# Optimization experiments

Measured on AMD Instinct MI355X. Metric: run time of the kernel, lower is better.

The kernel has to match this reference:

```python
import jax, jax.numpy as jnp
import numpy as np

H, KVH, HD = 16, 8, 64
EPS = 1e-6
SCALING = HD ** -0.5


def _rms_norm(x, w):
    # RMSNorm over last dim (head_dim)
    var = jnp.mean(x * x, axis=-1, keepdims=True)
    return x * jax.lax.rsqrt(var + EPS) * w


def _rotate_half(x):
    x1, x2 = jnp.split(x, 2, axis=-1)
    return jnp.concatenate([-x2, x1], axis=-1)


def setup_inputs() -> dict:
    key = jax.random.key(0)
    ks = jax.random.split(key, 12)
    B, Q, CTX, HID = 1, 2048, 2048, 1024
    NB, T = 32, 64  # Q == NB * T
    TOTAL = CTX + Q
    inp = {}
    inp["hidden_states"] = jax.random.normal(ks[0], (B, Q, HID), jnp.float32)
    inp["target_hidden"] = jax.random.normal(ks[1], (B, CTX, HID), jnp.float32)
    pos = jnp.arange(TOTAL, dtype=jnp.float32)[:, None]
    inv = 1.0 / (10000.0 ** (jnp.arange(0, HD, 2, dtype=jnp.float32) / HD))
    ang = pos * inv[None, :]
    emb = jnp.concatenate([ang, ang], axis=-1)
    inp["cos"] = jnp.cos(emb)[None]  # [B, TOTAL, HD]
    inp["sin"] = jnp.sin(emb)[None]
    inp["attention_mask"] = jnp.zeros((B, 1, Q, TOTAL), jnp.float32)
    s = 0.02
    inp["Wq"] = jax.random.normal(ks[2], (HID, H * HD), jnp.float32) * s
    inp["Wk"] = jax.random.normal(ks[3], (HID, KVH * HD), jnp.float32) * s
    inp["Wv"] = jax.random.normal(ks[4], (HID, KVH * HD), jnp.float32) * s
    inp["Wo"] = jax.random.normal(ks[5], (H * HD, HID), jnp.float32) * s
    inp["q_norm_w"] = jnp.ones((HD,), jnp.float32)
    inp["k_norm_w"] = jnp.ones((HD,), jnp.float32)
    inp["tree_bias"] = jax.random.normal(ks[6], (64, H), jnp.float32) * s
    inp["relation_map"] = jax.random.randint(ks[7], (B, NB, T, T), 0, 64, jnp.int32)
    return inp


def reference(hidden_states, target_hidden, cos, sin, attention_mask,
              Wq, Wk, Wv, Wo, q_norm_w, k_norm_w, tree_bias, relation_map):
    B, Q, HID = hidden_states.shape
    CTX = target_hidden.shape[1]
    TOTAL = CTX + Q
    NB, T = relation_map.shape[1], relation_map.shape[2]
    groups = H // KVH

    q = (hidden_states @ Wq).reshape(B, Q, H, HD)
    k_ctx = target_hidden @ Wk
    k_noise = hidden_states @ Wk
    v_ctx = target_hidden @ Wv
    v_noise = hidden_states @ Wv
    k = jnp.concatenate([k_ctx, k_noise], axis=1).reshape(B, TOTAL, KVH, HD)
    v = jnp.concatenate([v_ctx, v_noise], axis=1).reshape(B, TOTAL, KVH, HD)

    q = _rms_norm(q, q_norm_w).transpose(0, 2, 1, 3)  # [B,H,Q,HD]
    k = _rms_norm(k, k_norm_w).transpose(0, 2, 1, 3)  # [B,KVH,TOTAL,HD]
    v = v.transpose(0, 2, 1, 3)

    cos_b = cos[:, None]  # [B,1,TOTAL,HD]
    sin_b = sin[:, None]
    q = q * cos_b[..., -Q:, :] + _rotate_half(q) * sin_b[..., -Q:, :]
    k = k * cos_b + _rotate_half(k) * sin_b

    # GQA: repeat kv heads
    k = jnp.repeat(k, groups, axis=1)  # [B,H,TOTAL,HD]
    v = jnp.repeat(v, groups, axis=1)

    scores = jnp.einsum('bhqd,bhkd->bhqk', q, k) * SCALING  # [B,H,Q,TOTAL]
    scores = scores + attention_mask

    # tree positional bias: block-diagonal (same tree) on the noise-noise block
    bias = tree_bias[relation_map]                 # [B,NB,T,T,H]
    bias = jnp.transpose(bias, (0, 4, 1, 2, 3))    # [B,H,NB,T,T]
    s_noise = scores[..., CTX:].reshape(B, H, NB, T, NB, T)
    idx = jnp.arange(NB)
    s_noise = s_noise.at[:, :, idx, :, idx, :].add(jnp.transpose(bias, (2, 0, 1, 3, 4)))
    scores = jnp.concatenate([scores[..., :CTX], s_noise.reshape(B, H, Q, Q)], axis=-1)

    attn = jax.nn.softmax(scores, axis=-1)
    out = jnp.einsum('bhqk,bhkd->bhqd', attn, v)   # [B,H,Q,HD]
    out = out.transpose(0, 2, 1, 3).reshape(B, Q, H * HD)
    return out @ Wo
```

## Files before the change

kernel.cpp:

```cpp
#include <hip/hip_runtime.h>
#include <hip/hip_bf16.h>

typedef __bf16 bf16x8 __attribute__((ext_vector_type(8)));
typedef float  f32x4  __attribute__((ext_vector_type(4)));

__device__ inline unsigned short f2bf(float f) {
    unsigned int u = __float_as_uint(f);
    u += 0x7fffu + ((u >> 16) & 1u);
    return (unsigned short)(u >> 16);
}
__device__ inline float bf2f(unsigned int s) {
    return __uint_as_float(s << 16);
}
__device__ inline unsigned int pk2bf(float a, float b) {
    __hip_bfloat162 h = __float22bfloat162_rn(make_float2(a, b));
    union { __hip_bfloat162 h; unsigned int u; } cv;
    cv.h = h;
    return cv.u;
}
__device__ inline f32x4 mfma16(bf16x8 a, bf16x8 b, f32x4 c) {
    return __builtin_amdgcn_mfma_f32_16x16x32_bf16(a, b, c, 0, 0, 0);
}
__device__ inline void gload_lds16(const void* g, void* l) {
    __builtin_amdgcn_global_load_lds(
        (const __attribute__((address_space(1))) void*)g,
        (__attribute__((address_space(3))) void*)l, 16, 0, 0);
}

__global__ __launch_bounds__(256) void prep1(const float* __restrict__ th, const float* __restrict__ hs,
                                             const float* __restrict__ Wk, const float* __restrict__ Wv,
                                             const float* __restrict__ Wq, const float* __restrict__ Wo,
                                             unsigned short* __restrict__ X,
                                             unsigned short* __restrict__ Wkvt,
                                             unsigned short* __restrict__ Wqt,
                                             unsigned short* __restrict__ Wot) {
    __shared__ float t[64][65];
    int bx = blockIdx.x, tid = threadIdx.x;
    if (bx < 4096) {
        int i = bx * 256 + tid;
        const int n4 = 2048 * 1024 / 4;
        float4 v = (i < n4) ? ((const float4*)th)[i] : ((const float4*)hs)[i - n4];
        ((uint2*)X)[i] = make_uint2(pk2bf(v.x, v.y), pk2bf(v.z, v.w));
        return;
    }
    int t4 = bx - 4096;
    const float* in; unsigned short* out; int in_rs, xt, yt;
    if (t4 < 256)      { in = Wq; out = Wqt; in_rs = 1024; xt = t4 & 15; yt = t4 >> 4; }
    else if (t4 < 512) { t4 -= 256; in = Wo; out = Wot; in_rs = 1024; xt = t4 & 15; yt = t4 >> 4; }
    else if (t4 < 640) { t4 -= 512; in = Wk; out = Wkvt; in_rs = 512; xt = t4 & 7; yt = t4 >> 3; }
    else               { t4 -= 640; in = Wv; out = Wkvt + (size_t)512 * 1024; in_rs = 512; xt = t4 & 7; yt = t4 >> 3; }
    int r0 = yt * 64, c0b = xt * 64;
    int rr = tid >> 4, c4 = (tid & 15) * 4;
#pragma unroll
    for (int i = 0; i < 4; i++) {
        int r = rr + 16 * i;
        float4 v = *(const float4*)&in[(size_t)(r0 + r) * in_rs + c0b + c4];
        t[c4][r] = v.x; t[c4 + 1][r] = v.y; t[c4 + 2][r] = v.z; t[c4 + 3][r] = v.w;
    }
    __syncthreads();
#pragma unroll
    for (int i = 0; i < 4; i++) {
        int cc = rr + 16 * i;
        *(uint2*)&out[(size_t)(c0b + cc) * 1024 + r0 + c4] =
            make_uint2(pk2bf(t[cc][c4], t[cc][c4 + 1]), pk2bf(t[cc][c4 + 2], t[cc][c4 + 3]));
    }
}

union GemmLds {
    struct { unsigned short A[2][128 * 64]; unsigned short B[2][64 * 64]; } s;
    unsigned short Ost[128 * 72];
};

__device__ __forceinline__ void gemm_bk64(const unsigned short* __restrict__ A,
                                          const unsigned short* __restrict__ Bt,
                                          int m0, int n0,
                                          unsigned short* __restrict__ dstBf, int dstStride,
                                          const float* __restrict__ nw,
                                          const float* __restrict__ cosb,
                                          const float* __restrict__ sinb,
                                          int posBase, float scale,
                                          unsigned short* __restrict__ vtrDst,
                                          GemmLds* u) {
    int tid = threadIdx.x, wave = tid >> 6, lane = tid & 63, quad = lane >> 4, l16 = lane & 15;
    f32x4 acc[2][4] = {};

    int drow = lane >> 3;
    int sch = ((lane & 7) ^ drow) * 8;
    const unsigned short* AgB = A + (size_t)(m0 + wave * 32 + drow) * 1024 + sch;
    const unsigned short* BgB = Bt + (size_t)(n0 + wave * 16 + drow) * 1024 + sch;

    auto dma = [&](int k0, int b) {
#pragma unroll
        for (int ii = 0; ii < 4; ii++)
            gload_lds16(AgB + (size_t)ii * 8 * 1024 + k0, &u->s.A[b][(wave * 32 + ii * 8) * 64]);
#pragma unroll
        for (int jj = 0; jj < 2; jj++)
            gload_lds16(BgB + (size_t)jj * 8 * 1024 + k0, &u->s.B[b][(wave * 16 + jj * 8) * 64]);
    };
    dma(0, 0);

    for (int kt = 0; kt < 16; kt++) {
        int b = kt & 1;
        __syncthreads();
        if (kt < 15) dma((kt + 1) * 64, b ^ 1);
#pragma unroll
        for (int kk = 0; kk < 2; kk++) {
            int co = ((kk * 4 + quad) ^ (l16 & 7)) * 8;
            bf16x8 af0 = *(const bf16x8*)&u->s.A[b][(wave * 32 + l16) * 64 + co];
            bf16x8 af1 = *(const bf16x8*)&u->s.A[b][(wave * 32 + 16 + l16) * 64 + co];
            bf16x8 bq[4];
#pragma unroll
            for (int ng = 0; ng < 4; ng++)
                bq[ng] = *(const bf16x8*)&u->s.B[b][(ng * 16 + l16) * 64 + co];
#pragma unroll
            for (int ng = 0; ng < 4; ng++) {
                acc[0][ng] = mfma16(af0, bq[ng], acc[0][ng]);
                acc[1][ng] = mfma16(af1, bq[ng], acc[1][ng]);
            }
        }
    }

    __syncthreads();
    unsigned short* Ost = u->Ost;
    int c0 = l16, c1 = 16 + l16, c2 = 32 + l16, c3 = 48 + l16;
    if (nw) {
        float w0 = nw[c0], w1 = nw[c1], w2 = nw[c2], w3 = nw[c3];
#pragma unroll
        for (int i = 0; i < 2; i++) {
            float s[4];
#pragma unroll
            for (int r = 0; r < 4; r++)
                s[r] = acc[i][0][r] * acc[i][0][r] + acc[i][1][r] * acc[i][1][r] +
                       acc[i][2][r] * acc[i][2][r] + acc[i][3][r] * acc[i][3][r];
#pragma unroll
            for (int m = 1; m <= 8; m <<= 1) {
#pragma unroll
                for (int r = 0; r < 4; r++) s[r] += __shfl_xor(s[r], m);
            }
#pragma unroll
            for (int r = 0; r < 4; r++) {
                float rn = rsqrtf(s[r] * (1.0f / 64.0f) + 1e-6f);
                int row = wave * 32 + i * 16 + quad * 4 + r;
                size_t pos = (size_t)(posBase + m0 + row) * 64;
                float x0 = acc[i][0][r] * rn * w0, x1 = acc[i][1][r] * rn * w1;
                float x2 = acc[i][2][r] * rn * w2, x3 = acc[i][3][r] * rn * w3;
                float y0 = fmaf(x0, cosb[pos + c0], -x2 * sinb[pos + c0]) * scale;
                float y1 = fmaf(x1, cosb[pos + c1], -x3 * sinb[pos + c1]) * scale;
                float y2 = fmaf(x2, cosb[pos + c2],  x0 * sinb[pos + c2]) * scale;
                float y3 = fmaf(x3, cosb[pos + c3],  x1 * sinb[pos + c3]) * scale;
                Ost[row * 72 + c0] = f2bf(y0);
                Ost[row * 72 + c1] = f2bf(y1);
                Ost[row * 72 + c2] = f2bf(y2);
                Ost[row * 72 + c3] = f2bf(y3);
            }
        }
    } else {
#pragma unroll
        for (int i = 0; i < 2; i++)
#pragma unroll
            for (int r = 0; r < 4; r++) {
                int row = wave * 32 + i * 16 + quad * 4 + r;
                Ost[row * 72 + c0] = f2bf(acc[i][0][r]);
                Ost[row * 72 + c1] = f2bf(acc[i][1][r]);
                Ost[row * 72 + c2] = f2bf(acc[i][2][r]);
                Ost[row * 72 + c3] = f2bf(acc[i][3][r]);
            }
    }
    __syncthreads();
    if (vtrDst) {
        int d = tid >> 2, kseg = tid & 3;
        unsigned short* vrow = vtrDst + (size_t)d * 4096 + m0 + kseg * 32;
#pragma unroll
        for (int c = 0; c < 4; c++) {
            int kb = kseg * 32 + c * 8;
            uint4 w;
            w.x = (unsigned int)Ost[(kb + 0) * 72 + d] | ((unsigned int)Ost[(kb + 1) * 72 + d] << 16);
            w.y = (unsigned int)Ost[(kb + 2) * 72 + d] | ((unsigned int)Ost[(kb + 3) * 72 + d] << 16);
            w.z = (unsigned int)Ost[(kb + 4) * 72 + d] | ((unsigned int)Ost[(kb + 5) * 72 + d] << 16);
            w.w = (unsigned int)Ost[(kb + 6) * 72 + d] | ((unsigned int)Ost[(kb + 7) * 72 + d] << 16);
            *(uint4*)(vrow + c * 8) = w;
        }
        return;
    }
    int row = tid >> 3, c = (tid & 7) * 8;
#pragma unroll
    for (int i = 0; i < 4; i++) {
        int rr = row + 32 * i;
        uint4 val = *(uint4*)&Ost[rr * 72 + c];
        *(uint4*)&dstBf[(size_t)(m0 + rr) * dstStride + c] = val;
    }
}

__global__ __launch_bounds__(256) void gemm_qkv(const unsigned short* __restrict__ X,
                                                const unsigned short* __restrict__ Wkvt,
                                                const unsigned short* __restrict__ Wqt,
                                                const float* __restrict__ qnw,
                                                const float* __restrict__ knw,
                                                const float* __restrict__ cosb,
                                                const float* __restrict__ sinb,
                                                unsigned short* __restrict__ Qb,
                                                unsigned short* __restrict__ Kb,
                                                unsigned short* __restrict__ Vtr) {
    __shared__ GemmLds u;
    int ny = blockIdx.x, bx = blockIdx.y;
    if (bx < 32) {
        if (ny < 8)
            gemm_bk64(X, Wkvt, bx * 128, ny * 64,
                      Kb + (size_t)ny * 4096 * 64, 64, knw, cosb, sinb, 0, 1.0f, nullptr, &u);
        else
            gemm_bk64(X, Wkvt, bx * 128, ny * 64,
                      nullptr, 0, nullptr, nullptr, nullptr, 0, 1.0f,
                      Vtr + (size_t)(ny - 8) * 64 * 4096, &u);
    } else {
        gemm_bk64(X + (size_t)2048 * 1024, Wqt, (bx - 32) * 128, ny * 64,
                  Qb + (size_t)ny * 2048 * 64, 64, qnw, cosb, sinb, 2048,
                  0.18033688011112042f, nullptr, &u);
    }
}

__global__ __launch_bounds__(256) void gemm_wo64(const unsigned short* __restrict__ A,
                                                 const unsigned short* __restrict__ Bt,
                                                 float* __restrict__ C) {
    __shared__ struct { unsigned short A[2][4096]; unsigned short B[2][4096]; } u;
    int m0 = blockIdx.x * 64, n0 = blockIdx.y * 64;
    int tid = threadIdx.x, wave = tid >> 6, lane = tid & 63, quad = lane >> 4, l16 = lane & 15;
    f32x4 acc[4] = {};

    int drow = lane >> 3;
    int sch = ((lane & 7) ^ drow) * 8;
    const unsigned short* Ag0 = A + (size_t)(m0 + wave * 16 + drow) * 1024 + sch;
    const unsigned short* Bg0 = Bt + (size_t)(n0 + wave * 16 + drow) * 1024 + sch;

    auto dma = [&](int k0, int b) {
        gload_lds16(Ag0 + k0, &u.A[b][(wave * 16) * 64]);
        gload_lds16(Ag0 + (size_t)8 * 1024 + k0, &u.A[b][(wave * 16 + 8) * 64]);
        gload_lds16(Bg0 + k0, &u.B[b][(wave * 16) * 64]);
        gload_lds16(Bg0 + (size_t)8 * 1024 + k0, &u.B[b][(wave * 16 + 8) * 64]);
    };
    dma(0, 0);

    for (int kt = 0; kt < 16; kt++) {
        int b = kt & 1;
        __syncthreads();
        if (kt < 15) dma((kt + 1) * 64, b ^ 1);
#pragma unroll
        for (int kk = 0; kk < 2; kk++) {
            int co = ((kk * 4 + quad) ^ (l16 & 7)) * 8;
            bf16x8 af = *(const bf16x8*)&u.A[b][(wave * 16 + l16) * 64 + co];
#pragma unroll
            for (int ng = 0; ng < 4; ng++) {
                bf16x8 bq = *(const bf16x8*)&u.B[b][(ng * 16 + l16) * 64 + co];
                acc[ng] = mfma16(af, bq, acc[ng]);
            }
        }
    }
#pragma unroll
    for (int j = 0; j < 4; j++) {
        int n = n0 + j * 16 + l16;
#pragma unroll
        for (int r = 0; r < 4; r++)
            C[(size_t)(m0 + wave * 16 + quad * 4 + r) * 1024 + n] = acc[j][r];
    }
}

__global__ __launch_bounds__(256, 4) void attn5(const unsigned short* __restrict__ Qb,
                                                const unsigned short* __restrict__ Kb,
                                                const unsigned short* __restrict__ Vt,
                                                const int* __restrict__ relmap,
                                                const float* __restrict__ tree_bias,
                                                unsigned short* __restrict__ Opart,
                                                float* __restrict__ Lpart) {
    __shared__ alignas(16) union {
        struct { unsigned short K[2][4096]; unsigned short V[4096]; unsigned short P[4][2048]; } s;
        unsigned short O[128 * 72];
    } u;

    int qt = blockIdx.x, h = blockIdx.y, ks = blockIdx.z, kvh = h >> 1;
    int tid = threadIdx.x, wave = tid >> 6, lane = tid & 63, quad = lane >> 4, l16 = lane & 15;

    bf16x8 qf[2][2];
#pragma unroll
    for (int qg = 0; qg < 2; qg++) {
        int q = qt * 128 + wave * 32 + qg * 16 + l16;
        const unsigned short* qp = Qb + ((size_t)h * 2048 + q) * 64 + quad * 8;
        qf[qg][0] = *(const bf16x8*)qp;
        qf[qg][1] = *(const bf16x8*)(qp + 32);
    }
    f32x4 o[4][2] = {};
    f32x4 lacc[2] = {};
    union { unsigned short us[8]; bf16x8 v; } one_u;
#pragma unroll
    for (int i = 0; i < 8; i++) one_u.us[i] = 0x3F80;
    const bf16x8 ones = one_u.v;

    int drow = lane >> 3;
    int sch = ((lane & 7) ^ drow) * 8;
    const unsigned short* KgB = Kb + ((size_t)kvh * 4096 + ks * 1024) * 64;
    const unsigned short* VgB = Vt + (size_t)kvh * 64 * 4096 + ks * 1024;
    int r0 = wave * 16, r1 = r0 + 8;
    const unsigned short* Kg0 = KgB + (size_t)(r0 + drow) * 64 + sch;
    const unsigned short* Kg1 = KgB + (size_t)(r1 + drow) * 64 + sch;
    const unsigned short* Vg0 = VgB + (size_t)(r0 + drow) * 4096 + sch;
    const unsigned short* Vg1 = VgB + (size_t)(r1 + drow) * 4096 + sch;

    gload_lds16(Kg0, &u.s.K[0][r0 * 64]);
    gload_lds16(Kg1, &u.s.K[0][r1 * 64]);

    unsigned short* pw = &u.s.P[wave][0];
    int sw = l16 & 7;
    int psw = (l16 & 7) * 2;
    int nb = 2 * qt + (wave >> 1);
    int bias_kt = 32 + nb - ks * 16;
    const float LOG2E = 1.4426950408889634f;

    for (int kt = 0; kt < 16; kt++) {
        int b = kt & 1;
        __syncthreads();
        if (kt + 1 < 16) {
            gload_lds16(Kg0 + (kt + 1) * 4096, &u.s.K[b ^ 1][r0 * 64]);
            gload_lds16(Kg1 + (kt + 1) * 4096, &u.s.K[b ^ 1][r1 * 64]);
        }
        gload_lds16(Vg0 + kt * 64, &u.s.V[r0 * 64]);
        gload_lds16(Vg1 + kt * 64, &u.s.V[r1 * 64]);

#pragma unroll
        for (int g = 0; g < 4; g++) {
            int krow = (g * 16 + l16) * 64;
            bf16x8 kf0 = *(const bf16x8*)&u.s.K[b][krow + ((quad ^ sw) * 8)];
            bf16x8 kf1 = *(const bf16x8*)&u.s.K[b][krow + (((4 + quad) ^ sw) * 8)];
            float pv[2][4];
#pragma unroll
            for (int qg = 0; qg < 2; qg++) {
                f32x4 s = {};
                s = mfma16(kf0, qf[qg][0], s);
                s = mfma16(kf1, qf[qg][1], s);
#pragma unroll
                for (int r = 0; r < 4; r++) pv[qg][r] = s[r];
            }
            if (kt == bias_kt) {
#pragma unroll
                for (int qg = 0; qg < 2; qg++)
#pragma unroll
                    for (int r = 0; r < 4; r++) {
                        int t1 = (wave & 1) * 32 + qg * 16 + l16;
                        int t2 = g * 16 + quad * 4 + r;
                        int rel = relmap[nb * 4096 + t1 * 64 + t2];
                        pv[qg][r] += tree_bias[rel * 16 + h] * LOG2E;
                    }
            }
#pragma unroll
            for (int qg = 0; qg < 2; qg++) {
                float p0 = __builtin_amdgcn_exp2f(pv[qg][0]);
                float p1 = __builtin_amdgcn_exp2f(pv[qg][1]);
                float p2 = __builtin_amdgcn_exp2f(pv[qg][2]);
                float p3 = __builtin_amdgcn_exp2f(pv[qg][3]);
                *(uint2*)&pw[(qg * 16 + l16) * 64 + (((g * 4 + quad) ^ psw) * 4)] =
                    make_uint2(pk2bf(p0, p1), pk2bf(p2, p3));
            }
        }
        __syncthreads();

        bf16x8 pf[2][2];
#pragma unroll
        for (int qg = 0; qg < 2; qg++) {
            pf[qg][0] = *(const bf16x8*)&pw[(qg * 16 + l16) * 64 + (((quad * 2) ^ psw) * 4)];
            pf[qg][1] = *(const bf16x8*)&pw[(qg * 16 + l16) * 64 + (((8 + quad * 2) ^ psw) * 4)];
            lacc[qg] = mfma16(ones, pf[qg][0], lacc[qg]);
            lacc[qg] = mfma16(ones, pf[qg][1], lacc[qg]);
        }
#pragma unroll
        for (int dg = 0; dg < 4; dg++) {
            int vrow = (dg * 16 + l16) * 64;
            bf16x8 vf0 = *(const bf16x8*)&u.s.V[vrow + ((quad ^ sw) * 8)];
            bf16x8 vf1 = *(const bf16x8*)&u.s.V[vrow + (((4 + quad) ^ sw) * 8)];
#pragma unroll
            for (int qg = 0; qg < 2; qg++) {
                o[dg][qg] = mfma16(vf0, pf[qg][0], o[dg][qg]);
                o[dg][qg] = mfma16(vf1, pf[qg][1], o[dg][qg]);
            }
        }
    }
    __syncthreads();

    float lv0 = lacc[0][0], lv1 = lacc[1][0];
#pragma unroll
    for (int qg = 0; qg < 2; qg++) {
        int qlocal = wave * 32 + qg * 16 + l16;
#pragma unroll
        for (int dg = 0; dg < 4; dg++) {
            f32x4 ov = o[dg][qg];
            *(uint2*)&u.O[qlocal * 72 + dg * 16 + quad * 4] =
                make_uint2(pk2bf(ov[0], ov[1]), pk2bf(ov[2], ov[3]));
        }
        if (quad == 0)
            Lpart[((size_t)ks * 16 + h) * 2048 + qt * 128 + qlocal] = qg ? lv1 : lv0;
    }
    __syncthreads();
    int row = tid >> 3, c = (tid & 7) * 8;
#pragma unroll
    for (int i = 0; i < 4; i++) {
        int rr = row + 32 * i;
        uint4 val = *(uint4*)&u.O[rr * 72 + c];
        size_t q = qt * 128 + rr;
        *(uint4*)&Opart[((size_t)ks * 2048 + q) * 1024 + h * 64 + c] = val;
    }
}

__global__ __launch_bounds__(256) void combine4(const unsigned short* __restrict__ Op,
                                                const float* __restrict__ Lp,
                                                unsigned short* __restrict__ AO) {
    int t = blockIdx.x * 256 + threadIdx.x;
    int q = t >> 7, h = (t >> 3) & 15, c8 = (t & 7) * 8;
    size_t base = ((size_t)q * 16 + h) * 64 + c8;
    float s[8] = {};
    float l = 0.0f;
#pragma unroll
    for (int ks = 0; ks < 4; ks++) {
        uint4 v = *(const uint4*)&Op[(size_t)ks * 2097152 + base];
        s[0] += bf2f(v.x & 0xffff); s[1] += bf2f(v.x >> 16);
        s[2] += bf2f(v.y & 0xffff); s[3] += bf2f(v.y >> 16);
        s[4] += bf2f(v.z & 0xffff); s[5] += bf2f(v.z >> 16);
        s[6] += bf2f(v.w & 0xffff); s[7] += bf2f(v.w >> 16);
        l += Lp[((size_t)ks * 16 + h) * 2048 + q];
    }
    float inv = 1.0f / l;
    uint4 r;
    r.x = pk2bf(s[0] * inv, s[1] * inv);
    r.y = pk2bf(s[2] * inv, s[3] * inv);
    r.z = pk2bf(s[4] * inv, s[5] * inv);
    r.w = pk2bf(s[6] * inv, s[7] * inv);
    *(uint4*)&AO[base] = r;
}

extern "C" void kernel_launch(void* const* d_in, const int* in_sizes, int n_in,
                              void* d_out, int out_size, void* d_ws, size_t ws_size,
                              hipStream_t stream) {
    const float* hs   = (const float*)d_in[0];
    const float* th   = (const float*)d_in[1];
    const float* cosb = (const float*)d_in[2];
    const float* sinb = (const float*)d_in[3];
    const float* Wq  = (const float*)d_in[5];
    const float* Wk  = (const float*)d_in[6];
    const float* Wv  = (const float*)d_in[7];
    const float* Wo  = (const float*)d_in[8];
    const float* qnw = (const float*)d_in[9];
    const float* knw = (const float*)d_in[10];
    const float* tb  = (const float*)d_in[11];
    const int*   rm  = (const int*)d_in[12];
    float* out = (float*)d_out;

    char* ws = (char*)d_ws;
    size_t off = 0;
    auto alloc = [&](size_t b) { char* p = ws + off; off += (b + 255) & ~(size_t)255; return p; };
    char*           pool  = alloc((size_t)16 * 1024 * 1024);
    unsigned short* X     = (unsigned short*)pool;
    unsigned short* Opart = (unsigned short*)pool;
    unsigned short* Wqt   = (unsigned short*)alloc((size_t)1024 * 1024 * 2);
    unsigned short* Wkvt  = (unsigned short*)alloc((size_t)1024 * 1024 * 2);
    unsigned short* Wot   = (unsigned short*)alloc((size_t)1024 * 1024 * 2);
    unsigned short* Qb    = (unsigned short*)alloc((size_t)16 * 2048 * 64 * 2);
    unsigned short* Kb    = (unsigned short*)alloc((size_t)8 * 4096 * 64 * 2);
    unsigned short* Vtr   = (unsigned short*)alloc((size_t)8 * 64 * 4096 * 2);
    unsigned short* AOb   = (unsigned short*)alloc((size_t)2048 * 1024 * 2);
    float*          Lpart = (float*)alloc((size_t)4 * 16 * 2048 * 4);

    prep1<<<4864, 256, 0, stream>>>(th, hs, Wk, Wv, Wq, Wo, X, Wkvt, Wqt, Wot);
    gemm_qkv<<<dim3(16, 48), 256, 0, stream>>>(X, Wkvt, Wqt, qnw, knw, cosb, sinb, Qb, Kb, Vtr);
    attn5<<<dim3(16, 16, 4), 256, 0, stream>>>(Qb, Kb, Vtr, rm, tb, Opart, Lpart);
    combine4<<<1024, 256, 0, stream>>>(Opart, Lpart, AOb);
    gemm_wo64<<<dim3(32, 16), 256, 0, stream>>>(AOb, Wot, out);
}
```

Measured before the change: 191.5 us.

## Fuse split-K combine into Wo GEMM and remap block order for locality

The separate combine kernel that merged the four split-K attention partials is removed. The Wo GEMM now loads the partial outputs and softmax denominators directly, sums and normalizes them in registers, and writes the bf16 A tile into LDS while MFMAs run on the other buffer. This drops one launch and the round trip through the intermediate AO buffer, but each of the 16 column-block CTAs now redoes the combine for its row block, so partial reads grow. Block indices in gemm_qkv and attn5 are also remapped into groups of 8 to improve L2 reuse.

Result: slower. 211.1 us (+10.2%).

```diff
diff --git a/kernel.cpp b/kernel.cpp
--- a/kernel.cpp
+++ b/kernel.cpp
@@ -202,7 +202,10 @@
                                                 unsigned short* __restrict__ Kb,
                                                 unsigned short* __restrict__ Vtr) {
     __shared__ GemmLds u;
-    int ny = blockIdx.x, bx = blockIdx.y;
+    int lin = blockIdx.x + (blockIdx.y << 4);
+    int xr = lin & 7, rem = lin >> 3;
+    int bx = xr + 8 * (rem >> 4);
+    int ny = rem & 15;
     if (bx < 32) {
         if (ny < 8)
             gemm_bk64(X, Wkvt, bx * 128, ny * 64,
@@ -218,9 +221,10 @@
     }
 }
 
-__global__ __launch_bounds__(256) void gemm_wo64(const unsigned short* __restrict__ A,
-                                                 const unsigned short* __restrict__ Bt,
-                                                 float* __restrict__ C) {
+__global__ __launch_bounds__(256) void gemm_wo_fused(const unsigned short* __restrict__ Op,
+                                                     const float* __restrict__ Lp,
+                                                     const unsigned short* __restrict__ Bt,
+                                                     float* __restrict__ C) {
     __shared__ struct { unsigned short A[2][4096]; unsigned short B[2][4096]; } u;
     int m0 = blockIdx.x * 64, n0 = blockIdx.y * 64;
     int tid = threadIdx.x, wave = tid >> 6, lane = tid & 63, quad = lane >> 4, l16 = lane & 15;
@@ -228,21 +232,65 @@
 
     int drow = lane >> 3;
     int sch = ((lane & 7) ^ drow) * 8;
-    const unsigned short* Ag0 = A + (size_t)(m0 + wave * 16 + drow) * 1024 + sch;
     const unsigned short* Bg0 = Bt + (size_t)(n0 + wave * 16 + drow) * 1024 + sch;
-
-    auto dma = [&](int k0, int b) {
-        gload_lds16(Ag0 + k0, &u.A[b][(wave * 16) * 64]);
-        gload_lds16(Ag0 + (size_t)8 * 1024 + k0, &u.A[b][(wave * 16 + 8) * 64]);
+    auto dmaB = [&](int k0, int b) {
         gload_lds16(Bg0 + k0, &u.B[b][(wave * 16) * 64]);
         gload_lds16(Bg0 + (size_t)8 * 1024 + k0, &u.B[b][(wave * 16 + 8) * 64]);
     };
-    dma(0, 0);
+
+    int ar = tid >> 2, aj = tid & 3;
+    size_t q = (size_t)(m0 + ar);
+    const unsigned short* apB = Op + q * 1024 + aj * 16;
+    int wr = ar & 7;
+    int adst0 = ar * 64 + (((aj * 2) ^ wr) * 8);
+    int adst1 = ar * 64 + (((aj * 2 + 1) ^ wr) * 8);
+
+    uint4 v[4][2];
+    float lsum;
+    auto loadA = [&](int kt) {
+#pragma unroll
+        for (int ks = 0; ks < 4; ks++) {
+            const unsigned short* p = apB + (size_t)ks * 2097152 + kt * 64;
+            v[ks][0] = *(const uint4*)p;
+            v[ks][1] = *(const uint4*)(p + 8);
+        }
+        lsum = Lp[kt * 2048 + q] + Lp[32768 + kt * 2048 + q] +
+               Lp[65536 + kt * 2048 + q] + Lp[98304 + kt * 2048 + q];
+    };
+    auto combineA = [&](int b) {
+        float linv = 1.0f / lsum;
+        float f[16];
+#pragma unroll
+        for (int i = 0; i < 16; i++) f[i] = 0.0f;
+#pragma unroll
+        for (int ks = 0; ks < 4; ks++) {
+            const unsigned int* w = (const unsigned int*)&v[ks][0];
+#pragma unroll
+            for (int j = 0; j < 8; j++) {
+                f[j * 2]     += bf2f(w[j] & 0xffff);
+                f[j * 2 + 1] += bf2f(w[j] >> 16);
+            }
+        }
+        uint4 w0, w1;
+        w0.x = pk2bf(f[0] * linv, f[1] * linv);   w0.y = pk2bf(f[2] * linv, f[3] * linv);
+        w0.z = pk2bf(f[4] * linv, f[5] * linv);   w0.w = pk2bf(f[6] * linv, f[7] * linv);
+        w1.x = pk2bf(f[8] * linv, f[9] * linv);   w1.y = pk2bf(f[10] * linv, f[11] * linv);
+        w1.z = pk2bf(f[12] * linv, f[13] * linv); w1.w = pk2bf(f[14] * linv, f[15] * linv);
+        *(uint4*)&u.A[b][adst0] = w0;
+        *(uint4*)&u.A[b][adst1] = w1;
+    };
+
+    dmaB(0, 0);
+    loadA(0);
+    combineA(0);
 
     for (int kt = 0; kt < 16; kt++) {
         int b = kt & 1;
         __syncthreads();
-        if (kt < 15) dma((kt + 1) * 64, b ^ 1);
+        if (kt < 15) {
+            dmaB((kt + 1) * 64, b ^ 1);
+            loadA(kt + 1);
+        }
 #pragma unroll
         for (int kk = 0; kk < 2; kk++) {
             int co = ((kk * 4 + quad) ^ (l16 & 7)) * 8;
@@ -253,6 +301,7 @@
                 acc[ng] = mfma16(af, bq, acc[ng]);
             }
         }
+        if (kt < 15) combineA(b ^ 1);
     }
 #pragma unroll
     for (int j = 0; j < 4; j++) {
@@ -275,7 +324,11 @@
         unsigned short O[128 * 72];
     } u;
 
-    int qt = blockIdx.x, h = blockIdx.y, ks = blockIdx.z, kvh = h >> 1;
+    int lin = blockIdx.x + (blockIdx.y << 4) + (blockIdx.z << 8);
+    int xr = lin & 7, rem = lin >> 3;
+    int g = xr + 8 * (rem >> 4);
+    int qt = rem & 15;
+    int h = g >> 2, ks = g & 3, kvh = h >> 1;
     int tid = threadIdx.x, wave = tid >> 6, lane = tid & 63, quad = lane >> 4, l16 = lane & 15;
 
     bf16x8 qf[2][2];
@@ -324,8 +377,8 @@
         gload_lds16(Vg1 + kt * 64, &u.s.V[r1 * 64]);
 
 #pragma unroll
-        for (int g = 0; g < 4; g++) {
-            int krow = (g * 16 + l16) * 64;
+        for (int g2 = 0; g2 < 4; g2++) {
+            int krow = (g2 * 16 + l16) * 64;
             bf16x8 kf0 = *(const bf16x8*)&u.s.K[b][krow + ((quad ^ sw) * 8)];
             bf16x8 kf1 = *(const bf16x8*)&u.s.K[b][krow + (((4 + quad) ^ sw) * 8)];
             float pv[2][4];
@@ -343,7 +396,7 @@
 #pragma unroll
                     for (int r = 0; r < 4; r++) {
                         int t1 = (wave & 1) * 32 + qg * 16 + l16;
-                        int t2 = g * 16 + quad * 4 + r;
+                        int t2 = g2 * 16 + quad * 4 + r;
                         int rel = relmap[nb * 4096 + t1 * 64 + t2];
                         pv[qg][r] += tree_bias[rel * 16 + h] * LOG2E;
                     }
@@ -354,7 +407,7 @@
                 float p1 = __builtin_amdgcn_exp2f(pv[qg][1]);
                 float p2 = __builtin_amdgcn_exp2f(pv[qg][2]);
                 float p3 = __builtin_amdgcn_exp2f(pv[qg][3]);
-                *(uint2*)&pw[(qg * 16 + l16) * 64 + (((g * 4 + quad) ^ psw) * 4)] =
+                *(uint2*)&pw[(qg * 16 + l16) * 64 + (((g2 * 4 + quad) ^ psw) * 4)] =
                     make_uint2(pk2bf(p0, p1), pk2bf(p2, p3));
             }
         }
@@ -404,32 +457,6 @@
         size_t q = qt * 128 + rr;
         *(uint4*)&Opart[((size_t)ks * 2048 + q) * 1024 + h * 64 + c] = val;
     }
-}
-
-__global__ __launch_bounds__(256) void combine4(const unsigned short* __restrict__ Op,
-                                                const float* __restrict__ Lp,
-                                                unsigned short* __restrict__ AO) {
-    int t = blockIdx.x * 256 + threadIdx.x;
-    int q = t >> 7, h = (t >> 3) & 15, c8 = (t & 7) * 8;
-    size_t base = ((size_t)q * 16 + h) * 64 + c8;
-    float s[8] = {};
-    float l = 0.0f;
-#pragma unroll
-    for (int ks = 0; ks < 4; ks++) {
-        uint4 v = *(const uint4*)&Op[(size_t)ks * 2097152 + base];
-        s[0] += bf2f(v.x & 0xffff); s[1] += bf2f(v.x >> 16);
-        s[2] += bf2f(v.y & 0xffff); s[3] += bf2f(v.y >> 16);
-        s[4] += bf2f(v.z & 0xffff); s[5] += bf2f(v.z >> 16);
-        s[6] += bf2f(v.w & 0xffff); s[7] += bf2f(v.w >> 16);
-        l += Lp[((size_t)ks * 16 + h) * 2048 + q];
-    }
-    float inv = 1.0f / l;
-    uint4 r;
-    r.x = pk2bf(s[0] * inv, s[1] * inv);
-    r.y = pk2bf(s[2] * inv, s[3] * inv);
-    r.z = pk2bf(s[4] * inv, s[5] * inv);
-    r.w = pk2bf(s[6] * inv, s[7] * inv);
-    *(uint4*)&AO[base] = r;
 }
 
 extern "C" void kernel_launch(void* const* d_in, const int* in_sizes, int n_in,
@@ -461,12 +488,10 @@
     unsigned short* Qb    = (unsigned short*)alloc((size_t)16 * 2048 * 64 * 2);
     unsigned short* Kb    = (unsigned short*)alloc((size_t)8 * 4096 * 64 * 2);
     unsigned short* Vtr   = (unsigned short*)alloc((size_t)8 * 64 * 4096 * 2);
-    unsigned short* AOb   = (unsigned short*)alloc((size_t)2048 * 1024 * 2);
     float*          Lpart = (float*)alloc((size_t)4 * 16 * 2048 * 4);
 
     prep1<<<4864, 256, 0, stream>>>(th, hs, Wk, Wv, Wq, Wo, X, Wkvt, Wqt, Wot);
     gemm_qkv<<<dim3(16, 48), 256, 0, stream>>>(X, Wkvt, Wqt, qnw, knw, cosb, sinb, Qb, Kb, Vtr);
     attn5<<<dim3(16, 16, 4), 256, 0, stream>>>(Qb, Kb, Vtr, rm, tb, Opart, Lpart);
-    combine4<<<1024, 256, 0, stream>>>(Opart, Lpart, AOb);
-    gemm_wo64<<<dim3(32, 16), 256, 0, stream>>>(AOb, Wot, out);
-}
+    gemm_wo_fused<<<dim3(32, 16), 256, 0, stream>>>(Opart, Lpart, Wot, out);
+}
```
